# Kernel optimization log

Hardware: AMD Instinct MI355X
Metric: run time of the kernel (lower is better)

## Reference

```python
import jax, jax.numpy as jnp
import numpy as np

P, M, MD = 1024, 64, 16      # polynomials, monomials per poly, monomial dim
D, H, DH = 512, 8, 64        # embed dim, heads, head dim
L, FF, HID = 4, 2048, 1024   # transformer depth, ffn width, deepsets hidden
K = 2048                     # number of selectable (row, col) pairs
EPS = 1e-5


def setup_inputs() -> dict:
    key = jax.random.key(0)
    ks = iter(jax.random.split(key, 40))

    def w(shape, s=0.02):
        return jax.random.normal(next(ks), shape, dtype=jnp.float32) * s

    inp = {
        "ideal": jax.random.normal(next(ks), (P, M, MD), dtype=jnp.float32),
        "rows": jax.random.randint(next(ks), (K,), 0, P, dtype=jnp.int32),
        "cols": jax.random.randint(next(ks), (K,), 0, P, dtype=jnp.int32),
        # MonomialEmbedder
        "Wm": w((D, MD), 0.1), "bm": jnp.zeros((D,), jnp.float32),
        # PolynomialEmbedder (DeepSets): phi then sum-pool then rho (relu after every layer)
        "W_phi1": w((HID, D)), "b_phi1": jnp.zeros((HID,), jnp.float32),
        "W_phi2": w((HID, HID)), "b_phi2": jnp.zeros((HID,), jnp.float32),
        "W_rho1": w((HID, HID)), "b_rho1": jnp.zeros((HID,), jnp.float32),
        "W_rho2": w((D, HID)), "b_rho2": jnp.zeros((D,), jnp.float32),
        # Transformer stack (stacked over L layers)
        "Wq": w((L, D, D)), "bq": jnp.zeros((L, D), jnp.float32),
        "Wk": w((L, D, D)), "bk": jnp.zeros((L, D), jnp.float32),
        "Wv": w((L, D, D)), "bv": jnp.zeros((L, D), jnp.float32),
        "Wo": w((L, D, D)), "bo": jnp.zeros((L, D), jnp.float32),
        "ln1_w": jnp.ones((L, D), jnp.float32), "ln1_b": jnp.zeros((L, D), jnp.float32),
        "W1": w((L, FF, D)), "b1": jnp.zeros((L, FF), jnp.float32),
        "W2": w((L, D, FF)), "b2": jnp.zeros((L, D), jnp.float32),
        "ln2_w": jnp.ones((L, D), jnp.float32), "ln2_b": jnp.zeros((L, D), jnp.float32),
    }
    return inp


def _layernorm(x, w, b):
    mu = x.mean(-1, keepdims=True)
    var = ((x - mu) ** 2).mean(-1, keepdims=True)
    return (x - mu) / jnp.sqrt(var + EPS) * w + b


def reference(ideal, rows, cols, Wm, bm, W_phi1, b_phi1, W_phi2, b_phi2,
              W_rho1, b_rho1, W_rho2, b_rho2, Wq, bq, Wk, bk, Wv, bv, Wo, bo,
              ln1_w, ln1_b, W1, b1, W2, b2, ln2_w, ln2_b):
    n_poly = ideal.shape[0]
    # Monomial embedding: linear + relu  [P, M, D]
    h = jax.nn.relu(jnp.einsum('pmd,ed->pme', ideal, Wm) + bm)
    # DeepSets phi (relu each layer)
    h = jax.nn.relu(jnp.einsum('pme,he->pmh', h, W_phi1) + b_phi1)
    h = jax.nn.relu(jnp.einsum('pmh,gh->pmg', h, W_phi2) + b_phi2)
    # Sum-pool over monomials, then rho (relu each layer incl. last)
    s = h.sum(axis=1)                                  # [P, HID]
    s = jax.nn.relu(s @ W_rho1.T + b_rho1)
    x = jax.nn.relu(s @ W_rho2.T + b_rho2)             # [P, D]

    scale = 1.0 / jnp.sqrt(jnp.float32(DH))
    for l in range(L):
        q = (x @ Wq[l].T + bq[l]).reshape(n_poly, H, DH)
        k = (x @ Wk[l].T + bk[l]).reshape(n_poly, H, DH)
        v = (x @ Wv[l].T + bv[l]).reshape(n_poly, H, DH)
        scores = jnp.einsum('qhd,khd->hqk', q, k) * scale   # [H, P, P]
        attn = jax.nn.softmax(scores, axis=-1)
        o = jnp.einsum('hqk,khd->qhd', attn, v).reshape(n_poly, D)
        o = o @ Wo[l].T + bo[l]
        x = _layernorm(x + o, ln1_w[l], ln1_b[l])
        m = jax.nn.relu(x @ W1[l].T + b1[l]) @ W2[l].T + b2[l]
        x = _layernorm(x + m, ln2_w[l], ln2_b[l])

    values = x @ x.T                                   # [P, P]
    mask = jnp.full((n_poly, n_poly), -jnp.inf, dtype=values.dtype)
    mask = mask.at[rows, cols].set(0.0)
    return (values + mask).flatten()
```

## Files before the change

kernel.cpp:

```cpp
#include <hip/hip_runtime.h>
#include <hip/hip_bf16.h>

#define NP    1024
#define NM    64
#define MD_   16
#define D_    512
#define NH    8
#define DH_   64
#define NL    4
#define FF_   2048
#define HID_  1024
#define NK    2048
#define EPS_  1e-5f

typedef __attribute__((ext_vector_type(8))) short short8;
typedef __attribute__((ext_vector_type(4))) float f32x4;

static __device__ __forceinline__ unsigned short f2bf(float f) {
    __hip_bfloat16 h = __float2bfloat16(f);
    return *reinterpret_cast<unsigned short*>(&h);
}
static __device__ __forceinline__ float bf2f(unsigned short u) {
    unsigned int x = ((unsigned int)u) << 16;
    return __uint_as_float(x);
}

__global__ __launch_bounds__(256) void cvt_all(
    const float* __restrict__ s0, const float* __restrict__ s1,
    const float* __restrict__ s2, const float* __restrict__ s3,
    const float* __restrict__ s4, const float* __restrict__ s5,
    const float* __restrict__ s6,
    unsigned short* __restrict__ d0, unsigned short* __restrict__ d1,
    unsigned short* __restrict__ d2, unsigned short* __restrict__ d3,
    unsigned short* __restrict__ d4, unsigned short* __restrict__ d5,
    unsigned short* __restrict__ d6)
{
    const int i = blockIdx.x * 256 + threadIdx.x;
    const float* src; unsigned short* dst; int l;
    if      (i <  131072) { src = s0; dst = d0; l = i; }
    else if (i <  393216) { src = s1; dst = d1; l = i -  131072; }
    else if (i <  655360) { src = s2; dst = d2; l = i -  393216; }
    else if (i <  786432) { src = s3; dst = d3; l = i -  655360; }
    else if (i < 1048576) { src = s4; dst = d4; l = i -  786432; }
    else if (i < 2097152) { src = s5; dst = d5; l = i - 1048576; }
    else                  { src = s6; dst = d6; l = i - 2097152; }
    float4 v = *(const float4*)(src + (size_t)l * 4);
    ushort4 o;
    o.x = f2bf(v.x); o.y = f2bf(v.y); o.z = f2bf(v.z); o.w = f2bf(v.w);
    *(ushort4*)(dst + (size_t)l * 4) = o;
}

__global__ __launch_bounds__(256) void cvt_bf16_kernel(
    const float* __restrict__ in, unsigned short* __restrict__ out, int n4)
{
    const int i = blockIdx.x * 256 + threadIdx.x;
    if (i < n4) {
        float4 v = *(const float4*)(in + (size_t)i * 4);
        ushort4 o;
        o.x = f2bf(v.x); o.y = f2bf(v.y); o.z = f2bf(v.z); o.w = f2bf(v.w);
        *(ushort4*)(out + (size_t)i * 4) = o;
    }
}

__global__ __launch_bounds__(256) void cvt_pad64(
    const float* __restrict__ in, unsigned short* __restrict__ out, int nrows)
{
    const int tid = threadIdx.x;
    const int row = blockIdx.x * 32 + (tid >> 3);
    if (row >= nrows) return;
    const int c8 = (tid & 7) * 8;
    ushort4 o0 = {0, 0, 0, 0}, o1 = {0, 0, 0, 0};
    if (c8 < 16) {
        float4 a = *(const float4*)(in + (size_t)row * 16 + c8);
        float4 b = *(const float4*)(in + (size_t)row * 16 + c8 + 4);
        o0.x = f2bf(a.x); o0.y = f2bf(a.y); o0.z = f2bf(a.z); o0.w = f2bf(a.w);
        o1.x = f2bf(b.x); o1.y = f2bf(b.y); o1.z = f2bf(b.z); o1.w = f2bf(b.w);
    }
    *(ushort4*)(out + (size_t)row * 64 + c8) = o0;
    *(ushort4*)(out + (size_t)row * 64 + c8 + 4) = o1;
}

__global__ __launch_bounds__(256) void cvt_qkv_kernel(
    const float* __restrict__ Wq, const float* __restrict__ Wk,
    const float* __restrict__ Wv, const float* __restrict__ bq,
    const float* __restrict__ bk, const float* __restrict__ bv,
    unsigned short* __restrict__ w_qkv, float* __restrict__ b_qkvc)
{
    const int part = blockIdx.y;
    const int l    = blockIdx.z;
    const float* src  = (part == 0 ? Wq : part == 1 ? Wk : Wv) + (size_t)l * D_ * D_;
    const float* bsrc = (part == 0 ? bq : part == 1 ? bk : bv) + l * D_;
    unsigned short* dst = w_qkv + (size_t)l * 1536 * D_ + (size_t)part * 512 * D_;
    const int i = blockIdx.x * 256 + threadIdx.x;
    float4 v = *(const float4*)(src + (size_t)i * 4);
    ushort4 o;
    o.x = f2bf(v.x); o.y = f2bf(v.y); o.z = f2bf(v.z); o.w = f2bf(v.w);
    *(ushort4*)(dst + (size_t)i * 4) = o;
    if (blockIdx.x == 0) {
        b_qkvc[l * 1536 + part * 512 + threadIdx.x * 2]     = bsrc[threadIdx.x * 2];
        b_qkvc[l * 1536 + part * 512 + threadIdx.x * 2 + 1] = bsrc[threadIdx.x * 2 + 1];
    }
}

template<int ISSUES>
static __device__ __forceinline__ void stage_tile(
    const unsigned short* __restrict__ src, int ld,
    unsigned short* lds, int wave, int lane)
{
    const int rl  = lane >> 3;
    const int sw8 = (((lane & 7) ^ rl) << 3);
#pragma unroll
    for (int i = 0; i < ISSUES; ++i) {
        const int rbase = i * 32 + wave * 8;
        const unsigned short* g = src + (size_t)(rbase + rl) * ld + sw8;
        unsigned short* l = lds + rbase * 64;
        __builtin_amdgcn_global_load_lds(
            (const __attribute__((address_space(1))) void*)g,
            (__attribute__((address_space(3))) void*)l, 16, 0, 0);
    }
}

template<int BM, int BN, int MODE, bool OUTF32, bool BIAS, bool RELU, bool POOL,
         bool RESID, bool TRANSV, bool DBUF>
__global__ __launch_bounds__(256) void mfma_nt(
    const unsigned short* __restrict__ A, long long aBatch, int lda,
    const unsigned short* __restrict__ W, long long bBatch, int ldb,
    const float* __restrict__ bias,
    const float* __restrict__ resid, int ldr,
    void* __restrict__ Cout, long long cBatch, int ldc,
    int K, float alpha, unsigned short* __restrict__ vTout)
{
    constexpr int BK = 64;
    constexpr int MI = BM / 32, NJ = BN / 32;
    __shared__ unsigned short Asl[(DBUF ? 2 : 1) * BM * BK];
    __shared__ unsigned short Bsl[(DBUF ? 2 : 1) * BN * BK];

    const int tid  = threadIdx.x;
    const int wave = tid >> 6, lane = tid & 63;
    const int wm = wave >> 1, wn = wave & 1;
    int row0, col0;
    if (MODE == 2) {
        const int f = blockIdx.x;
        const int lo = f & 7, mid = (f >> 3) & 7, hi = f >> 6;
        row0 = (hi * 8 + lo) * BM;
        col0 = mid * BN;
    } else {
        row0 = blockIdx.y * BM;
        col0 = blockIdx.x * BN;
    }
    const long long bz = blockIdx.z;
    A += bz * aBatch + (size_t)row0 * lda;
    W += bz * bBatch + (size_t)col0 * ldb;

    f32x4 acc[MI][NJ];
#pragma unroll
    for (int i = 0; i < MI; ++i)
#pragma unroll
        for (int j = 0; j < NJ; ++j) acc[i][j] = (f32x4){0.f, 0.f, 0.f, 0.f};

    if (DBUF) {
        stage_tile<MI>(A, lda, Asl, wave, lane);
        stage_tile<NJ>(W, ldb, Bsl, wave, lane);
        __syncthreads();
    }
    int cur = 0;
    for (int k0 = 0; k0 < K; k0 += BK) {
        const unsigned short *Ac, *Bc;
        if (DBUF) {
            if (k0 + BK < K) {
                stage_tile<MI>(A + k0 + BK, lda, Asl + (cur ^ 1) * BM * BK, wave, lane);
                stage_tile<NJ>(W + k0 + BK, ldb, Bsl + (cur ^ 1) * BN * BK, wave, lane);
            }
            Ac = Asl + cur * BM * BK;
            Bc = Bsl + cur * BN * BK;
        } else {
            stage_tile<MI>(A + k0, lda, Asl, wave, lane);
            stage_tile<NJ>(W + k0, ldb, Bsl, wave, lane);
            __syncthreads();
            Ac = Asl; Bc = Bsl;
        }
#pragma unroll
        for (int ks = 0; ks < 2; ++ks) {
            short8 a[MI], b[NJ];
            const int kbase = ks * 64 + (lane >> 4) * 16;
#pragma unroll
            for (int i = 0; i < MI; ++i) {
                const int ra = wm * (BM / 2) + i * 16 + (lane & 15);
                a[i] = *(const short8*)((const char*)Ac + ra * 128 + (kbase ^ ((ra & 7) << 4)));
            }
#pragma unroll
            for (int j = 0; j < NJ; ++j) {
                const int rb = wn * (BN / 2) + j * 16 + (lane & 15);
                b[j] = *(const short8*)((const char*)Bc + rb * 128 + (kbase ^ ((rb & 7) << 4)));
            }
#pragma unroll
            for (int i = 0; i < MI; ++i)
#pragma unroll
                for (int j = 0; j < NJ; ++j)
                    acc[i][j] = __builtin_amdgcn_mfma_f32_16x16x32_bf16(
                        a[i], b[j], acc[i][j], 0, 0, 0);
        }
        __syncthreads();
        cur ^= 1;
    }

    if (POOL) {
        float* red = (float*)Asl;
        red[tid] = 0.f;
        __syncthreads();
#pragma unroll
        for (int j = 0; j < NJ; ++j) {
            const int c = wn * (BN / 2) + j * 16 + (lane & 15);
            const float bi = BIAS ? bias[col0 + c] : 0.f;
            float s = 0.f;
#pragma unroll
            for (int i = 0; i < MI; ++i) {
                f32x4 v = acc[i][j];
#pragma unroll
                for (int r2 = 0; r2 < 4; ++r2) {
                    float val = v[r2] * alpha + bi;
                    if (RELU) val = fmaxf(val, 0.f);
                    s += val;
                }
            }
            atomicAdd(&red[wm * BN + c], s);
        }
        __syncthreads();
        float* C = (float*)Cout + bz * cBatch;
        const int pm = tid >> 7, c = tid & 127;
        C[(size_t)(row0 / 64 + pm) * ldc + col0 + c] = red[pm * BN + c];
    } else if (TRANSV && col0 >= 1024) {
        unsigned short* tr = Asl;
#pragma unroll
        for (int i = 0; i < MI; ++i) {
            const int rr = wm * (BM / 2) + i * 16 + (lane >> 4) * 4;
#pragma unroll
            for (int j = 0; j < NJ; ++j) {
                const int c = wn * (BN / 2) + j * 16 + (lane & 15);
                const float bi = BIAS ? bias[col0 + c] : 0.f;
                f32x4 v = acc[i][j];
#pragma unroll
                for (int r2 = 0; r2 < 4; ++r2)
                    tr[(rr + r2) * BN + c] = f2bf(v[r2] * alpha + bi);
            }
        }
        __syncthreads();
        const int c  = tid >> 2;
        const int r4 = (tid & 3) * 16;
        ushort4 o[4];
#pragma unroll
        for (int e = 0; e < 16; ++e)
            ((unsigned short*)o)[e] = tr[(r4 + e) * BN + c];
        unsigned short* dst = vTout + (size_t)(col0 - 1024 + c) * 1024 + row0 + r4;
        *(ushort4*)(dst + 0)  = o[0];
        *(ushort4*)(dst + 4)  = o[1];
        *(ushort4*)(dst + 8)  = o[2];
        *(ushort4*)(dst + 12) = o[3];
    } else {
        float* Cf = (float*)Cout + (OUTF32 ? bz * cBatch : 0);
        unsigned short* Cu = (unsigned short*)Cout + (OUTF32 ? 0 : bz * cBatch);
#pragma unroll
        for (int i = 0; i < MI; ++i) {
            const int rg = row0 + wm * (BM / 2) + i * 16 + (lane >> 4) * 4;
#pragma unroll
            for (int j = 0; j < NJ; ++j) {
                const int c = col0 + wn * (BN / 2) + j * 16 + (lane & 15);
                const float bi = BIAS ? bias[c] : 0.f;
                f32x4 v = acc[i][j];
#pragma unroll
                for (int r2 = 0; r2 < 4; ++r2) {
                    float val = v[r2] * alpha + bi;
                    if (RELU) val = fmaxf(val, 0.f);
                    if (RESID) val += resid[(size_t)(rg + r2) * ldr + c];
                    if (OUTF32) Cf[(size_t)(rg + r2) * ldc + c] = val;
                    else        Cu[(size_t)(rg + r2) * ldc + c] = f2bf(val);
                }
            }
        }
    }
}

__global__ __launch_bounds__(256) void flash_attn(
    const unsigned short* __restrict__ qkv,
    const unsigned short* __restrict__ vT,
    unsigned short* __restrict__ O)
{
    __shared__ unsigned short Qs[64 * 64];
    __shared__ unsigned short Ks[2][64 * 64];
    __shared__ unsigned short Vs[2][64 * 64];
    __shared__ unsigned short Ps[64 * 64];

    const int tid = threadIdx.x, wave = tid >> 6, lane = tid & 63;
    const int q0 = blockIdx.x * 64;
    const int h  = blockIdx.y;

    stage_tile<2>(qkv + (size_t)q0 * 1536 + h * 64, 1536, Qs, wave, lane);
    stage_tile<2>(qkv + 512 + h * 64, 1536, Ks[0], wave, lane);
    stage_tile<2>(vT + (size_t)(h * 64) * 1024, 1024, Vs[0], wave, lane);
    __syncthreads();

    f32x4 Oacc[4];
#pragma unroll
    for (int j = 0; j < 4; ++j) Oacc[j] = (f32x4){0.f, 0.f, 0.f, 0.f};
    float mrow[4] = {-1e30f, -1e30f, -1e30f, -1e30f};
    float lrow[4] = {0.f, 0.f, 0.f, 0.f};

    for (int kt = 0; kt < 16; ++kt) {
        if (kt < 15) {
            stage_tile<2>(qkv + 512 + (size_t)((kt + 1) * 64) * 1536 + h * 64, 1536,
                          Ks[(kt + 1) & 1], wave, lane);
            stage_tile<2>(vT + (size_t)(h * 64) * 1024 + (kt + 1) * 64, 1024,
                          Vs[(kt + 1) & 1], wave, lane);
        }
        const unsigned short* Kc = Ks[kt & 1];
        const unsigned short* Vc = Vs[kt & 1];

        f32x4 s[4];
#pragma unroll
        for (int j = 0; j < 4; ++j) s[j] = (f32x4){0.f, 0.f, 0.f, 0.f};
#pragma unroll
        for (int ks = 0; ks < 2; ++ks) {
            const int kbase = ks * 64 + (lane >> 4) * 16;
            const int ra = wave * 16 + (lane & 15);
            short8 aq = *(const short8*)((const char*)Qs + ra * 128 + (kbase ^ ((ra & 7) << 4)));
#pragma unroll
            for (int j = 0; j < 4; ++j) {
                const int rb = j * 16 + (lane & 15);
                short8 bk8 = *(const short8*)((const char*)Kc + rb * 128 + (kbase ^ ((rb & 7) << 4)));
                s[j] = __builtin_amdgcn_mfma_f32_16x16x32_bf16(aq, bk8, s[j], 0, 0, 0);
            }
        }

        float f[4];
#pragma unroll
        for (int r = 0; r < 4; ++r) {
            float mx = -1e30f;
#pragma unroll
            for (int j = 0; j < 4; ++j) { s[j][r] *= 0.125f; mx = fmaxf(mx, s[j][r]); }
#pragma unroll
            for (int o = 1; o < 16; o <<= 1) mx = fmaxf(mx, __shfl_xor(mx, o));
            const float mn = fmaxf(mrow[r], mx);
            f[r] = expf(mrow[r] - mn);
            mrow[r] = mn;
            float sm = 0.f;
#pragma unroll
            for (int j = 0; j < 4; ++j) { s[j][r] = expf(s[j][r] - mn); sm += s[j][r]; }
#pragma unroll
            for (int o = 1; o < 16; o <<= 1) sm += __shfl_xor(sm, o);
            lrow[r] = lrow[r] * f[r] + sm;
        }
#pragma unroll
        for (int j = 0; j < 4; ++j)
#pragma unroll
            for (int r = 0; r < 4; ++r) Oacc[j][r] *= f[r];

#pragma unroll
        for (int j = 0; j < 4; ++j) {
            const int col = (lane & 15) + j * 16;
#pragma unroll
            for (int r = 0; r < 4; ++r) {
                const int row = wave * 16 + (lane >> 4) * 4 + r;
                *(unsigned short*)((char*)Ps + row * 128 + ((col * 2) ^ ((row & 7) << 4))) =
                    f2bf(s[j][r]);
            }
        }

#pragma unroll
        for (int ks = 0; ks < 2; ++ks) {
            const int kbase = ks * 64 + (lane >> 4) * 16;
            const int ra = wave * 16 + (lane & 15);
            short8 ap = *(const short8*)((const char*)Ps + ra * 128 + (kbase ^ ((ra & 7) << 4)));
#pragma unroll
            for (int j = 0; j < 4; ++j) {
                const int rb = j * 16 + (lane & 15);
                short8 bv8 = *(const short8*)((const char*)Vc + rb * 128 + (kbase ^ ((rb & 7) << 4)));
                Oacc[j] = __builtin_amdgcn_mfma_f32_16x16x32_bf16(ap, bv8, Oacc[j], 0, 0, 0);
            }
        }
        __syncthreads();
    }

    float linv[4];
#pragma unroll
    for (int r = 0; r < 4; ++r) linv[r] = 1.0f / lrow[r];
#pragma unroll
    for (int j = 0; j < 4; ++j) {
        const int c = h * 64 + j * 16 + (lane & 15);
#pragma unroll
        for (int r = 0; r < 4; ++r) {
            const int row = q0 + wave * 16 + (lane >> 4) * 4 + r;
            O[(size_t)row * D_ + c] = f2bf(Oacc[j][r] * linv[r]);
        }
    }
}

__global__ __launch_bounds__(64) void ln_kernel(
    const float* __restrict__ y, const float* __restrict__ w,
    const float* __restrict__ b, float* __restrict__ x,
    unsigned short* __restrict__ xb)
{
    const int row = blockIdx.x;
    const int lane = threadIdx.x;
    const float* yr = y + (long long)row * 512;
    float4 v0 = *(const float4*)(yr + lane * 8);
    float4 v1 = *(const float4*)(yr + lane * 8 + 4);
    float vals[8] = {v0.x, v0.y, v0.z, v0.w, v1.x, v1.y, v1.z, v1.w};
    float s = 0.f;
#pragma unroll
    for (int j = 0; j < 8; ++j) s += vals[j];
#pragma unroll
    for (int o = 32; o >= 1; o >>= 1) s += __shfl_xor(s, o);
    const float mu = s * (1.f / 512.f);
    float q = 0.f;
#pragma unroll
    for (int j = 0; j < 8; ++j) { float d = vals[j] - mu; q += d * d; }
#pragma unroll
    for (int o = 32; o >= 1; o >>= 1) q += __shfl_xor(q, o);
    const float inv = 1.0f / sqrtf(q * (1.f / 512.f) + EPS_);
    float ov[8];
#pragma unroll
    for (int j = 0; j < 8; ++j)
        ov[j] = (vals[j] - mu) * inv * w[lane * 8 + j] + b[lane * 8 + j];
    float4 o0 = {ov[0], ov[1], ov[2], ov[3]};
    float4 o1 = {ov[4], ov[5], ov[6], ov[7]};
    *(float4*)(x + (long long)row * 512 + lane * 8) = o0;
    *(float4*)(x + (long long)row * 512 + lane * 8 + 4) = o1;
    ushort4 u0, u1;
    u0.x = f2bf(ov[0]); u0.y = f2bf(ov[1]); u0.z = f2bf(ov[2]); u0.w = f2bf(ov[3]);
    u1.x = f2bf(ov[4]); u1.y = f2bf(ov[5]); u1.z = f2bf(ov[6]); u1.w = f2bf(ov[7]);
    *(ushort4*)(xb + (long long)row * 512 + lane * 8) = u0;
    *(ushort4*)(xb + (long long)row * 512 + lane * 8 + 4) = u1;
}

__global__ __launch_bounds__(64) void ln_sum4_kernel(
    const float* __restrict__ y4,
    const float* __restrict__ bias,
    const float* __restrict__ w, const float* __restrict__ b,
    float* __restrict__ x, unsigned short* __restrict__ xb)
{
    const int row = blockIdx.x;
    const int lane = threadIdx.x;
    const size_t off = (size_t)row * 512 + lane * 8;
    float vals[8];
#pragma unroll
    for (int j = 0; j < 8; ++j) vals[j] = x[off + j] + bias[lane * 8 + j];
#pragma unroll
    for (int z = 0; z < 4; ++z) {
        float4 p0 = *(const float4*)(y4 + (size_t)z * 524288 + off);
        float4 p1 = *(const float4*)(y4 + (size_t)z * 524288 + off + 4);
        vals[0] += p0.x; vals[1] += p0.y; vals[2] += p0.z; vals[3] += p0.w;
        vals[4] += p1.x; vals[5] += p1.y; vals[6] += p1.z; vals[7] += p1.w;
    }
    float s = 0.f;
#pragma unroll
    for (int j = 0; j < 8; ++j) s += vals[j];
#pragma unroll
    for (int o = 32; o >= 1; o >>= 1) s += __shfl_xor(s, o);
    const float mu = s * (1.f / 512.f);
    float q = 0.f;
#pragma unroll
    for (int j = 0; j < 8; ++j) { float d = vals[j] - mu; q += d * d; }
#pragma unroll
    for (int o = 32; o >= 1; o >>= 1) q += __shfl_xor(q, o);
    const float inv = 1.0f / sqrtf(q * (1.f / 512.f) + EPS_);
    float ov[8];
#pragma unroll
    for (int j = 0; j < 8; ++j)
        ov[j] = (vals[j] - mu) * inv * w[lane * 8 + j] + b[lane * 8 + j];
    float4 o0 = {ov[0], ov[1], ov[2], ov[3]};
    float4 o1 = {ov[4], ov[5], ov[6], ov[7]};
    *(float4*)(x + off) = o0;
    *(float4*)(x + off + 4) = o1;
    ushort4 u0, u1;
    u0.x = f2bf(ov[0]); u0.y = f2bf(ov[1]); u0.z = f2bf(ov[2]); u0.w = f2bf(ov[3]);
    u1.x = f2bf(ov[4]); u1.y = f2bf(ov[5]); u1.z = f2bf(ov[6]); u1.w = f2bf(ov[7]);
    *(ushort4*)(xb + off) = u0;
    *(ushort4*)(xb + off + 4) = u1;
}

__global__ __launch_bounds__(256) void fill_sentinel_bf16(unsigned short* __restrict__ out)
{
    const long long i = (long long)blockIdx.x * blockDim.x + threadIdx.x;
    const unsigned int pat = 0xFBFFFBFFu;
    uint4 v = {pat, pat, pat, pat};
    *(uint4*)(out + i * 8) = v;
}

__global__ __launch_bounds__(256) void scatter_dot(
    const int* __restrict__ rows, const int* __restrict__ cols,
    const unsigned short* __restrict__ xb, __hip_bfloat16* __restrict__ out)
{
    const int k = blockIdx.x * 4 + (threadIdx.x >> 6);
    const int lane = threadIdx.x & 63;
    const int r = rows[k], c = cols[k];
    const unsigned short* xr = xb + (size_t)r * 512 + lane * 8;
    const unsigned short* xc = xb + (size_t)c * 512 + lane * 8;
    ushort4 a0 = *(const ushort4*)xr, a1 = *(const ushort4*)(xr + 4);
    ushort4 b0 = *(const ushort4*)xc, b1 = *(const ushort4*)(xc + 4);
    float s = bf2f(a0.x) * bf2f(b0.x) + bf2f(a0.y) * bf2f(b0.y) +
              bf2f(a0.z) * bf2f(b0.z) + bf2f(a0.w) * bf2f(b0.w) +
              bf2f(a1.x) * bf2f(b1.x) + bf2f(a1.y) * bf2f(b1.y) +
              bf2f(a1.z) * bf2f(b1.z) + bf2f(a1.w) * bf2f(b1.w);
#pragma unroll
    for (int o = 32; o >= 1; o >>= 1) s += __shfl_xor(s, o);
    if (lane == 0) {
        if (!(fabsf(s) < 1e30f)) s = 0.f;
        out[(size_t)r * 1024 + c] = __float2bfloat16(s);
    }
}

extern "C" void kernel_launch(void* const* d_in, const int* in_sizes, int n_in,
                              void* d_out, int out_size, void* d_ws, size_t ws_size,
                              hipStream_t stream)
{
    const float* ideal  = (const float*)d_in[0];
    const int*   rows   = (const int*)d_in[1];
    const int*   cols   = (const int*)d_in[2];
    const float* Wm     = (const float*)d_in[3];
    const float* bm     = (const float*)d_in[4];
    const float* Wphi1  = (const float*)d_in[5];
    const float* bphi1  = (const float*)d_in[6];
    const float* Wphi2  = (const float*)d_in[7];
    const float* bphi2  = (const float*)d_in[8];
    const float* Wrho1  = (const float*)d_in[9];
    const float* brho1  = (const float*)d_in[10];
    const float* Wrho2  = (const float*)d_in[11];
    const float* brho2  = (const float*)d_in[12];
    const float* Wq     = (const float*)d_in[13];
    const float* bq     = (const float*)d_in[14];
    const float* Wk     = (const float*)d_in[15];
    const float* bk     = (const float*)d_in[16];
    const float* Wv     = (const float*)d_in[17];
    const float* bv     = (const float*)d_in[18];
    const float* Wo     = (const float*)d_in[19];
    const float* bo     = (const float*)d_in[20];
    const float* ln1w   = (const float*)d_in[21];
    const float* ln1b   = (const float*)d_in[22];
    const float* W1     = (const float*)d_in[23];
    const float* b1     = (const float*)d_in[24];
    const float* W2     = (const float*)d_in[25];
    const float* b2     = (const float*)d_in[26];
    const float* ln2w   = (const float*)d_in[27];
    const float* ln2b   = (const float*)d_in[28];
    __hip_bfloat16* out = (__hip_bfloat16*)d_out;

    char* base = (char*)d_ws;
    unsigned short* w_phi1 = (unsigned short*)(base + (0ll  << 20));
    unsigned short* w_phi2 = (unsigned short*)(base + (1ll  << 20));
    unsigned short* w_rho1 = (unsigned short*)(base + (3ll  << 20));
    unsigned short* w_rho2 = (unsigned short*)(base + (5ll  << 20));
    unsigned short* w_qkv  = (unsigned short*)(base + (6ll  << 20));
    unsigned short* w_o    = (unsigned short*)(base + (12ll << 20));
    unsigned short* w_1    = (unsigned short*)(base + (14ll << 20));
    unsigned short* w_2    = (unsigned short*)(base + (22ll << 20));
    float*          b_qkvc = (float*)         (base + (30ll << 20));
    unsigned short* h0b    = (unsigned short*)(base + (31ll << 20));
    unsigned short* h1b    = (unsigned short*)(base + (95ll << 20));
    float*          sbuf   = (float*)         (base + (223ll << 20));
    unsigned short* id_pad = (unsigned short*)(base + (227ll << 20));
    unsigned short* wm_pad = (unsigned short*)(base + (236ll << 20));
    unsigned short* sb_b   = (unsigned short*)(base + (31ll << 20));
    unsigned short* tb_b   = (unsigned short*)(base + (33ll << 20));
    float*          xbuf   = (float*)         (base + (35ll << 20));
    unsigned short* xb     = (unsigned short*)(base + (37ll << 20));
    float*          ybuf   = (float*)         (base + (38ll << 20));
    unsigned short* qkvb   = (unsigned short*)(base + (40ll << 20));
    unsigned short* vT     = (unsigned short*)(base + (43ll << 20));
    unsigned short* ob     = (unsigned short*)(base + (44ll << 20));
    unsigned short* ffnt   = (unsigned short*)(base + (45ll << 20));
    float*          ysplit = (float*)         (base + (49ll << 20));

    fill_sentinel_bf16<<<512, 256, 0, stream>>>((unsigned short*)out);

    cvt_all<<<12288, 256, 0, stream>>>(Wphi1, Wphi2, Wrho1, Wrho2, Wo, W1, W2,
                                       w_phi1, w_phi2, w_rho1, w_rho2, w_o, w_1, w_2);
    cvt_qkv_kernel<<<dim3(256, 3, NL), 256, 0, stream>>>(Wq, Wk, Wv, bq, bk, bv,
                                                          w_qkv, b_qkvc);
    cvt_pad64<<<2048, 256, 0, stream>>>(ideal, id_pad, NP * NM);
    cvt_pad64<<<16, 256, 0, stream>>>(Wm, wm_pad, D_);

    mfma_nt<128, 128, 0, false, true, true, false, false, false, false><<<dim3(4, 512), 256, 0, stream>>>(
        id_pad, 0, 64, wm_pad, 0, 64, bm, nullptr, 0, h0b, 0, D_, 64, 1.0f, nullptr);
    mfma_nt<128, 128, 2, false, true, true, false, false, false, false><<<4096, 256, 0, stream>>>(
        h0b, 0, D_, w_phi1, 0, D_, bphi1, nullptr, 0, h1b, 0, HID_, D_, 1.0f, nullptr);
    mfma_nt<128, 128, 2, true, true, true, true, false, false, false><<<4096, 256, 0, stream>>>(
        h1b, 0, HID_, w_phi2, 0, HID_, bphi2, nullptr, 0, sbuf, 0, HID_, HID_, 1.0f, nullptr);

    cvt_bf16_kernel<<<1024, 256, 0, stream>>>(sbuf, sb_b, 262144);
    mfma_nt<64, 64, 0, false, true, true, false, false, false, true><<<dim3(16, 16), 256, 0, stream>>>(
        sb_b, 0, HID_, w_rho1, 0, HID_, brho1, nullptr, 0, tb_b, 0, HID_, HID_, 1.0f, nullptr);
    mfma_nt<64, 64, 0, true, true, true, false, false, false, true><<<dim3(8, 16), 256, 0, stream>>>(
        tb_b, 0, HID_, w_rho2, 0, HID_, brho2, nullptr, 0, xbuf, 0, D_, HID_, 1.0f, nullptr);
    cvt_bf16_kernel<<<512, 256, 0, stream>>>(xbuf, xb, 131072);

    for (int l = 0; l < NL; ++l) {
        mfma_nt<64, 64, 0, false, true, false, false, false, true, true><<<dim3(24, 16), 256, 0, stream>>>(
            xb, 0, D_, w_qkv + (long long)l * 1536 * D_, 0, D_, b_qkvc + l * 1536,
            nullptr, 0, qkvb, 0, 1536, D_, 1.0f, vT);
        flash_attn<<<dim3(16, NH), 256, 0, stream>>>(qkvb, vT, ob);
        mfma_nt<64, 64, 0, true, true, false, false, true, false, true><<<dim3(8, 16), 256, 0, stream>>>(
            ob, 0, D_, w_o + (long long)l * D_ * D_, 0, D_, bo + l * D_,
            xbuf, D_, ybuf, 0, D_, D_, 1.0f, nullptr);
        ln_kernel<<<NP, 64, 0, stream>>>(ybuf, ln1w + l * D_, ln1b + l * D_, xbuf, xb);
        mfma_nt<64, 64, 0, false, true, true, false, false, false, true><<<dim3(32, 16), 256, 0, stream>>>(
            xb, 0, D_, w_1 + (long long)l * FF_ * D_, 0, D_, b1 + l * FF_,
            nullptr, 0, ffnt, 0, FF_, D_, 1.0f, nullptr);
        mfma_nt<64, 64, 0, true, false, false, false, false, false, true><<<dim3(8, 16, 4), 256, 0, stream>>>(
            ffnt, 512, FF_, w_2 + (long long)l * D_ * FF_, 512, FF_, nullptr,
            nullptr, 0, ysplit, 524288, D_, 512, 1.0f, nullptr);
        ln_sum4_kernel<<<NP, 64, 0, stream>>>(ysplit, b2 + l * D_,
                                              ln2w + l * D_, ln2b + l * D_, xbuf, xb);
    }

    scatter_dot<<<NK / 4, 256, 0, stream>>>(rows, cols, xb, out);
}
```

Before: 646.3 us.

## Split attention over key halves, split-K Wo GEMM, and merge conversion kernels

Flash attention is split into two key-range partitions, each writing unnormalized fp32 partials plus row max/sum, and a new merge kernel combines them into bf16. The Wo projection becomes a split-K GEMM whose partials are reduced inside a generalized LayerNorm-sum kernel. All weight conversion and sentinel-fill kernels are fused into one launch, and the rho2 GEMM also writes the bf16 copy directly. The aim is more parallelism from the 128-block attention grid and fewer launches, at the cost of extra fp32 partial traffic and one added merge launch per layer.

```diff
diff --git a/kernel.cpp b/kernel.cpp
--- a/kernel.cpp
+++ b/kernel.cpp
@@ -25,29 +25,74 @@
     return __uint_as_float(x);
 }
 
-__global__ __launch_bounds__(256) void cvt_all(
-    const float* __restrict__ s0, const float* __restrict__ s1,
-    const float* __restrict__ s2, const float* __restrict__ s3,
-    const float* __restrict__ s4, const float* __restrict__ s5,
-    const float* __restrict__ s6,
-    unsigned short* __restrict__ d0, unsigned short* __restrict__ d1,
-    unsigned short* __restrict__ d2, unsigned short* __restrict__ d3,
-    unsigned short* __restrict__ d4, unsigned short* __restrict__ d5,
-    unsigned short* __restrict__ d6)
-{
-    const int i = blockIdx.x * 256 + threadIdx.x;
-    const float* src; unsigned short* dst; int l;
-    if      (i <  131072) { src = s0; dst = d0; l = i; }
-    else if (i <  393216) { src = s1; dst = d1; l = i -  131072; }
-    else if (i <  655360) { src = s2; dst = d2; l = i -  393216; }
-    else if (i <  786432) { src = s3; dst = d3; l = i -  655360; }
-    else if (i < 1048576) { src = s4; dst = d4; l = i -  786432; }
-    else if (i < 2097152) { src = s5; dst = d5; l = i - 1048576; }
-    else                  { src = s6; dst = d6; l = i - 2097152; }
-    float4 v = *(const float4*)(src + (size_t)l * 4);
-    ushort4 o;
-    o.x = f2bf(v.x); o.y = f2bf(v.y); o.z = f2bf(v.z); o.w = f2bf(v.w);
-    *(ushort4*)(dst + (size_t)l * 4) = o;
+__global__ __launch_bounds__(256) void mega_cvt(
+    const float* __restrict__ Wphi1, const float* __restrict__ Wphi2,
+    const float* __restrict__ Wrho1, const float* __restrict__ Wrho2,
+    const float* __restrict__ Wo,    const float* __restrict__ W1,
+    const float* __restrict__ W2,
+    unsigned short* __restrict__ w_phi1, unsigned short* __restrict__ w_phi2,
+    unsigned short* __restrict__ w_rho1, unsigned short* __restrict__ w_rho2,
+    unsigned short* __restrict__ w_o,    unsigned short* __restrict__ w_1,
+    unsigned short* __restrict__ w_2,
+    const float* __restrict__ Wq, const float* __restrict__ Wk,
+    const float* __restrict__ Wv, const float* __restrict__ bq,
+    const float* __restrict__ bk, const float* __restrict__ bv,
+    unsigned short* __restrict__ w_qkv, float* __restrict__ b_qkvc,
+    const float* __restrict__ ideal, unsigned short* __restrict__ id_pad,
+    const float* __restrict__ Wm,    unsigned short* __restrict__ wm_pad,
+    unsigned short* __restrict__ out)
+{
+    const int b = blockIdx.x, t = threadIdx.x;
+    if (b < 512) {
+        const long long i = (long long)b * 256 + t;
+        const unsigned int pat = 0xFBFFFBFFu;
+        uint4 v = {pat, pat, pat, pat};
+        *(uint4*)(out + i * 8) = v;
+    } else if (b < 12800) {
+        const int i = (b - 512) * 256 + t;
+        const float* src; unsigned short* dst; int l;
+        if      (i <  131072) { src = Wphi1; dst = w_phi1; l = i; }
+        else if (i <  393216) { src = Wphi2; dst = w_phi2; l = i -  131072; }
+        else if (i <  655360) { src = Wrho1; dst = w_rho1; l = i -  393216; }
+        else if (i <  786432) { src = Wrho2; dst = w_rho2; l = i -  655360; }
+        else if (i < 1048576) { src = Wo;    dst = w_o;    l = i -  786432; }
+        else if (i < 2097152) { src = W1;    dst = w_1;    l = i - 1048576; }
+        else                  { src = W2;    dst = w_2;    l = i - 2097152; }
+        float4 v = *(const float4*)(src + (size_t)l * 4);
+        ushort4 o;
+        o.x = f2bf(v.x); o.y = f2bf(v.y); o.z = f2bf(v.z); o.w = f2bf(v.w);
+        *(ushort4*)(dst + (size_t)l * 4) = o;
+    } else if (b < 15872) {
+        const int g = (b - 12800) >> 8;
+        const int inner = (b - 12800) & 255;
+        const int part = g % 3, l = g / 3;
+        const float* src  = (part == 0 ? Wq : part == 1 ? Wk : Wv) + (size_t)l * D_ * D_;
+        const float* bsrc = (part == 0 ? bq : part == 1 ? bk : bv) + l * D_;
+        unsigned short* dst = w_qkv + (size_t)l * 1536 * D_ + (size_t)part * 512 * D_;
+        const int i = inner * 256 + t;
+        float4 v = *(const float4*)(src + (size_t)i * 4);
+        ushort4 o;
+        o.x = f2bf(v.x); o.y = f2bf(v.y); o.z = f2bf(v.z); o.w = f2bf(v.w);
+        *(ushort4*)(dst + (size_t)i * 4) = o;
+        if (inner == 0) {
+            b_qkvc[l * 1536 + part * 512 + t * 2]     = bsrc[t * 2];
+            b_qkvc[l * 1536 + part * 512 + t * 2 + 1] = bsrc[t * 2 + 1];
+        }
+    } else {
+        const float* src; unsigned short* dst; int row;
+        if (b < 17920) { src = ideal; dst = id_pad; row = (b - 15872) * 32 + (t >> 3); }
+        else           { src = Wm;    dst = wm_pad; row = (b - 17920) * 32 + (t >> 3); }
+        const int c8 = (t & 7) * 8;
+        ushort4 o0 = {0, 0, 0, 0}, o1 = {0, 0, 0, 0};
+        if (c8 < 16) {
+            float4 a = *(const float4*)(src + (size_t)row * 16 + c8);
+            float4 bb = *(const float4*)(src + (size_t)row * 16 + c8 + 4);
+            o0.x = f2bf(a.x);  o0.y = f2bf(a.y);  o0.z = f2bf(a.z);  o0.w = f2bf(a.w);
+            o1.x = f2bf(bb.x); o1.y = f2bf(bb.y); o1.z = f2bf(bb.z); o1.w = f2bf(bb.w);
+        }
+        *(ushort4*)(dst + (size_t)row * 64 + c8) = o0;
+        *(ushort4*)(dst + (size_t)row * 64 + c8 + 4) = o1;
+    }
 }
 
 __global__ __launch_bounds__(256) void cvt_bf16_kernel(
@@ -59,46 +104,6 @@
         ushort4 o;
         o.x = f2bf(v.x); o.y = f2bf(v.y); o.z = f2bf(v.z); o.w = f2bf(v.w);
         *(ushort4*)(out + (size_t)i * 4) = o;
-    }
-}
-
-__global__ __launch_bounds__(256) void cvt_pad64(
-    const float* __restrict__ in, unsigned short* __restrict__ out, int nrows)
-{
-    const int tid = threadIdx.x;
-    const int row = blockIdx.x * 32 + (tid >> 3);
-    if (row >= nrows) return;
-    const int c8 = (tid & 7) * 8;
-    ushort4 o0 = {0, 0, 0, 0}, o1 = {0, 0, 0, 0};
-    if (c8 < 16) {
-        float4 a = *(const float4*)(in + (size_t)row * 16 + c8);
-        float4 b = *(const float4*)(in + (size_t)row * 16 + c8 + 4);
-        o0.x = f2bf(a.x); o0.y = f2bf(a.y); o0.z = f2bf(a.z); o0.w = f2bf(a.w);
-        o1.x = f2bf(b.x); o1.y = f2bf(b.y); o1.z = f2bf(b.z); o1.w = f2bf(b.w);
-    }
-    *(ushort4*)(out + (size_t)row * 64 + c8) = o0;
-    *(ushort4*)(out + (size_t)row * 64 + c8 + 4) = o1;
-}
-
-__global__ __launch_bounds__(256) void cvt_qkv_kernel(
-    const float* __restrict__ Wq, const float* __restrict__ Wk,
-    const float* __restrict__ Wv, const float* __restrict__ bq,
-    const float* __restrict__ bk, const float* __restrict__ bv,
-    unsigned short* __restrict__ w_qkv, float* __restrict__ b_qkvc)
-{
-    const int part = blockIdx.y;
-    const int l    = blockIdx.z;
-    const float* src  = (part == 0 ? Wq : part == 1 ? Wk : Wv) + (size_t)l * D_ * D_;
-    const float* bsrc = (part == 0 ? bq : part == 1 ? bk : bv) + l * D_;
-    unsigned short* dst = w_qkv + (size_t)l * 1536 * D_ + (size_t)part * 512 * D_;
-    const int i = blockIdx.x * 256 + threadIdx.x;
-    float4 v = *(const float4*)(src + (size_t)i * 4);
-    ushort4 o;
-    o.x = f2bf(v.x); o.y = f2bf(v.y); o.z = f2bf(v.z); o.w = f2bf(v.w);
-    *(ushort4*)(dst + (size_t)i * 4) = o;
-    if (blockIdx.x == 0) {
-        b_qkvc[l * 1536 + part * 512 + threadIdx.x * 2]     = bsrc[threadIdx.x * 2];
-        b_qkvc[l * 1536 + part * 512 + threadIdx.x * 2 + 1] = bsrc[threadIdx.x * 2 + 1];
     }
 }
 
@@ -121,7 +126,7 @@
 }
 
 template<int BM, int BN, int MODE, bool OUTF32, bool BIAS, bool RELU, bool POOL,
-         bool RESID, bool TRANSV, bool DBUF>
+         bool RESID, bool TRANSV, bool DBUF, bool BOTH>
 __global__ __launch_bounds__(256) void mfma_nt(
     const unsigned short* __restrict__ A, long long aBatch, int lda,
     const unsigned short* __restrict__ W, long long bBatch, int ldb,
@@ -272,8 +277,12 @@
                     float val = v[r2] * alpha + bi;
                     if (RELU) val = fmaxf(val, 0.f);
                     if (RESID) val += resid[(size_t)(rg + r2) * ldr + c];
-                    if (OUTF32) Cf[(size_t)(rg + r2) * ldc + c] = val;
-                    else        Cu[(size_t)(rg + r2) * ldc + c] = f2bf(val);
+                    if (OUTF32) {
+                        Cf[(size_t)(rg + r2) * ldc + c] = val;
+                        if (BOTH) vTout[(size_t)(rg + r2) * ldc + c] = f2bf(val);
+                    } else {
+                        Cu[(size_t)(rg + r2) * ldc + c] = f2bf(val);
+                    }
                 }
             }
         }
@@ -283,7 +292,8 @@
 __global__ __launch_bounds__(256) void flash_attn(
     const unsigned short* __restrict__ qkv,
     const unsigned short* __restrict__ vT,
-    unsigned short* __restrict__ O)
+    float* __restrict__ Of,
+    float* __restrict__ mlb)
 {
     __shared__ unsigned short Qs[64 * 64];
     __shared__ unsigned short Ks[2][64 * 64];
@@ -293,10 +303,12 @@
     const int tid = threadIdx.x, wave = tid >> 6, lane = tid & 63;
     const int q0 = blockIdx.x * 64;
     const int h  = blockIdx.y;
+    const int z  = blockIdx.z;
+    const int kt0 = z * 8;
 
     stage_tile<2>(qkv + (size_t)q0 * 1536 + h * 64, 1536, Qs, wave, lane);
-    stage_tile<2>(qkv + 512 + h * 64, 1536, Ks[0], wave, lane);
-    stage_tile<2>(vT + (size_t)(h * 64) * 1024, 1024, Vs[0], wave, lane);
+    stage_tile<2>(qkv + 512 + (size_t)(kt0 * 64) * 1536 + h * 64, 1536, Ks[0], wave, lane);
+    stage_tile<2>(vT + (size_t)(h * 64) * 1024 + kt0 * 64, 1024, Vs[0], wave, lane);
     __syncthreads();
 
     f32x4 Oacc[4];
@@ -305,11 +317,11 @@
     float mrow[4] = {-1e30f, -1e30f, -1e30f, -1e30f};
     float lrow[4] = {0.f, 0.f, 0.f, 0.f};
 
-    for (int kt = 0; kt < 16; ++kt) {
-        if (kt < 15) {
-            stage_tile<2>(qkv + 512 + (size_t)((kt + 1) * 64) * 1536 + h * 64, 1536,
+    for (int kt = 0; kt < 8; ++kt) {
+        if (kt < 7) {
+            stage_tile<2>(qkv + 512 + (size_t)((kt0 + kt + 1) * 64) * 1536 + h * 64, 1536,
                           Ks[(kt + 1) & 1], wave, lane);
-            stage_tile<2>(vT + (size_t)(h * 64) * 1024 + (kt + 1) * 64, 1024,
+            stage_tile<2>(vT + (size_t)(h * 64) * 1024 + (kt0 + kt + 1) * 64, 1024,
                           Vs[(kt + 1) & 1], wave, lane);
         }
         const unsigned short* Kc = Ks[kt & 1];
@@ -380,59 +392,62 @@
         __syncthreads();
     }
 
-    float linv[4];
-#pragma unroll
-    for (int r = 0; r < 4; ++r) linv[r] = 1.0f / lrow[r];
+    float* Oz = Of + (size_t)z * 524288;
 #pragma unroll
     for (int j = 0; j < 4; ++j) {
         const int c = h * 64 + j * 16 + (lane & 15);
 #pragma unroll
         for (int r = 0; r < 4; ++r) {
             const int row = q0 + wave * 16 + (lane >> 4) * 4 + r;
-            O[(size_t)row * D_ + c] = f2bf(Oacc[j][r] * linv[r]);
-        }
-    }
-}
-
-__global__ __launch_bounds__(64) void ln_kernel(
-    const float* __restrict__ y, const float* __restrict__ w,
-    const float* __restrict__ b, float* __restrict__ x,
-    unsigned short* __restrict__ xb)
-{
-    const int row = blockIdx.x;
-    const int lane = threadIdx.x;
-    const float* yr = y + (long long)row * 512;
-    float4 v0 = *(const float4*)(yr + lane * 8);
-    float4 v1 = *(const float4*)(yr + lane * 8 + 4);
-    float vals[8] = {v0.x, v0.y, v0.z, v0.w, v1.x, v1.y, v1.z, v1.w};
-    float s = 0.f;
-#pragma unroll
-    for (int j = 0; j < 8; ++j) s += vals[j];
-#pragma unroll
-    for (int o = 32; o >= 1; o >>= 1) s += __shfl_xor(s, o);
-    const float mu = s * (1.f / 512.f);
-    float q = 0.f;
-#pragma unroll
-    for (int j = 0; j < 8; ++j) { float d = vals[j] - mu; q += d * d; }
-#pragma unroll
-    for (int o = 32; o >= 1; o >>= 1) q += __shfl_xor(q, o);
-    const float inv = 1.0f / sqrtf(q * (1.f / 512.f) + EPS_);
-    float ov[8];
-#pragma unroll
-    for (int j = 0; j < 8; ++j)
-        ov[j] = (vals[j] - mu) * inv * w[lane * 8 + j] + b[lane * 8 + j];
-    float4 o0 = {ov[0], ov[1], ov[2], ov[3]};
-    float4 o1 = {ov[4], ov[5], ov[6], ov[7]};
-    *(float4*)(x + (long long)row * 512 + lane * 8) = o0;
-    *(float4*)(x + (long long)row * 512 + lane * 8 + 4) = o1;
-    ushort4 u0, u1;
-    u0.x = f2bf(ov[0]); u0.y = f2bf(ov[1]); u0.z = f2bf(ov[2]); u0.w = f2bf(ov[3]);
-    u1.x = f2bf(ov[4]); u1.y = f2bf(ov[5]); u1.z = f2bf(ov[6]); u1.w = f2bf(ov[7]);
-    *(ushort4*)(xb + (long long)row * 512 + lane * 8) = u0;
-    *(ushort4*)(xb + (long long)row * 512 + lane * 8 + 4) = u1;
-}
-
-__global__ __launch_bounds__(64) void ln_sum4_kernel(
+            Oz[(size_t)row * D_ + c] = Oacc[j][r];
+        }
+    }
+    if ((lane & 15) == 0 && h == 0) {  }
+    if ((lane & 15) == 0) {
+#pragma unroll
+        for (int r = 0; r < 4; ++r) {
+            const int row = q0 + wave * 16 + (lane >> 4) * 4 + r;
+            float* dst = mlb + (((size_t)z * NH + h) * 1024 + row) * 2;
+            dst[0] = mrow[r];
+            dst[1] = lrow[r];
+        }
+    }
+}
+
+__global__ __launch_bounds__(256) void flash_merge(
+    const float* __restrict__ Of, const float* __restrict__ mlb,
+    unsigned short* __restrict__ O)
+{
+    const int tid = threadIdx.x;
+    const int row = blockIdx.x * 4 + (tid >> 6);
+    const int lane = tid & 63;
+    const int d0 = lane * 8;
+    const int h = d0 >> 6;
+    const float* ml0 = mlb + (((size_t)0 * NH + h) * 1024 + row) * 2;
+    const float* ml1 = mlb + (((size_t)1 * NH + h) * 1024 + row) * 2;
+    const float m0 = ml0[0], l0 = ml0[1], m1 = ml1[0], l1 = ml1[1];
+    const float m = fmaxf(m0, m1);
+    const float a0 = expf(m0 - m), a1 = expf(m1 - m);
+    const float inv = 1.0f / (a0 * l0 + a1 * l1);
+    const float* p0 = Of + (size_t)row * D_ + d0;
+    const float* p1 = Of + 524288 + (size_t)row * D_ + d0;
+    float4 x0 = *(const float4*)p0, x1 = *(const float4*)(p0 + 4);
+    float4 y0 = *(const float4*)p1, y1 = *(const float4*)(p1 + 4);
+    ushort4 o0, o1;
+    o0.x = f2bf((a0 * x0.x + a1 * y0.x) * inv);
+    o0.y = f2bf((a0 * x0.y + a1 * y0.y) * inv);
+    o0.z = f2bf((a0 * x0.z + a1 * y0.z) * inv);
+    o0.w = f2bf((a0 * x0.w + a1 * y0.w) * inv);
+    o1.x = f2bf((a0 * x1.x + a1 * y1.x) * inv);
+    o1.y = f2bf((a0 * x1.y + a1 * y1.y) * inv);
+    o1.z = f2bf((a0 * x1.z + a1 * y1.z) * inv);
+    o1.w = f2bf((a0 * x1.w + a1 * y1.w) * inv);
+    *(ushort4*)(O + (size_t)row * D_ + d0) = o0;
+    *(ushort4*)(O + (size_t)row * D_ + d0 + 4) = o1;
+}
+
+template<int NZ>
+__global__ __launch_bounds__(64) void ln_sum_kernel(
     const float* __restrict__ y4,
     const float* __restrict__ bias,
     const float* __restrict__ w, const float* __restrict__ b,
@@ -445,7 +460,7 @@
 #pragma unroll
     for (int j = 0; j < 8; ++j) vals[j] = x[off + j] + bias[lane * 8 + j];
 #pragma unroll
-    for (int z = 0; z < 4; ++z) {
+    for (int z = 0; z < NZ; ++z) {
         float4 p0 = *(const float4*)(y4 + (size_t)z * 524288 + off);
         float4 p1 = *(const float4*)(y4 + (size_t)z * 524288 + off + 4);
         vals[0] += p0.x; vals[1] += p0.y; vals[2] += p0.z; vals[3] += p0.w;
@@ -476,14 +491,6 @@
     u1.x = f2bf(ov[4]); u1.y = f2bf(ov[5]); u1.z = f2bf(ov[6]); u1.w = f2bf(ov[7]);
     *(ushort4*)(xb + off) = u0;
     *(ushort4*)(xb + off + 4) = u1;
-}
-
-__global__ __launch_bounds__(256) void fill_sentinel_bf16(unsigned short* __restrict__ out)
-{
-    const long long i = (long long)blockIdx.x * blockDim.x + threadIdx.x;
-    const unsigned int pat = 0xFBFFFBFFu;
-    uint4 v = {pat, pat, pat, pat};
-    *(uint4*)(out + i * 8) = v;
 }
 
 __global__ __launch_bounds__(256) void scatter_dot(
@@ -563,53 +570,61 @@
     unsigned short* tb_b   = (unsigned short*)(base + (33ll << 20));
     float*          xbuf   = (float*)         (base + (35ll << 20));
     unsigned short* xb     = (unsigned short*)(base + (37ll << 20));
-    float*          ybuf   = (float*)         (base + (38ll << 20));
     unsigned short* qkvb   = (unsigned short*)(base + (40ll << 20));
     unsigned short* vT     = (unsigned short*)(base + (43ll << 20));
     unsigned short* ob     = (unsigned short*)(base + (44ll << 20));
     unsigned short* ffnt   = (unsigned short*)(base + (45ll << 20));
     float*          ysplit = (float*)         (base + (49ll << 20));
-
-    fill_sentinel_bf16<<<512, 256, 0, stream>>>((unsigned short*)out);
-
-    cvt_all<<<12288, 256, 0, stream>>>(Wphi1, Wphi2, Wrho1, Wrho2, Wo, W1, W2,
-                                       w_phi1, w_phi2, w_rho1, w_rho2, w_o, w_1, w_2);
-    cvt_qkv_kernel<<<dim3(256, 3, NL), 256, 0, stream>>>(Wq, Wk, Wv, bq, bk, bv,
-                                                          w_qkv, b_qkvc);
-    cvt_pad64<<<2048, 256, 0, stream>>>(ideal, id_pad, NP * NM);
-    cvt_pad64<<<16, 256, 0, stream>>>(Wm, wm_pad, D_);
-
-    mfma_nt<128, 128, 0, false, true, true, false, false, false, false><<<dim3(4, 512), 256, 0, stream>>>(
+    float*          Of     = (float*)         (base + (57ll << 20));
+    float*          mlb    = (float*)         (base + (61ll << 20));
+
+    mega_cvt<<<17936, 256, 0, stream>>>(
+        Wphi1, Wphi2, Wrho1, Wrho2, Wo, W1, W2,
+        w_phi1, w_phi2, w_rho1, w_rho2, w_o, w_1, w_2,
+        Wq, Wk, Wv, bq, bk, bv, w_qkv, b_qkvc,
+        ideal, id_pad, Wm, wm_pad, (unsigned short*)out);
+
+    mfma_nt<128, 128, 0, false, true, true, false, false, false, false, false>
+        <<<dim3(4, 512), 256, 0, stream>>>(
         id_pad, 0, 64, wm_pad, 0, 64, bm, nullptr, 0, h0b, 0, D_, 64, 1.0f, nullptr);
-    mfma_nt<128, 128, 2, false, true, true, false, false, false, false><<<4096, 256, 0, stream>>>(
+    mfma_nt<128, 128, 2, false, true, true, false, false, false, false, false>
+        <<<4096, 256, 0, stream>>>(
         h0b, 0, D_, w_phi1, 0, D_, bphi1, nullptr, 0, h1b, 0, HID_, D_, 1.0f, nullptr);
-    mfma_nt<128, 128, 2, true, true, true, true, false, false, false><<<4096, 256, 0, stream>>>(
+    mfma_nt<128, 128, 2, true, true, true, true, false, false, false, false>
+        <<<4096, 256, 0, stream>>>(
         h1b, 0, HID_, w_phi2, 0, HID_, bphi2, nullptr, 0, sbuf, 0, HID_, HID_, 1.0f, nullptr);
 
     cvt_bf16_kernel<<<1024, 256, 0, stream>>>(sbuf, sb_b, 262144);
-    mfma_nt<64, 64, 0, false, true, true, false, false, false, true><<<dim3(16, 16), 256, 0, stream>>>(
+    mfma_nt<64, 64, 0, false, true, true, false, false, false, true, false>
+        <<<dim3(16, 16), 256, 0, stream>>>(
         sb_b, 0, HID_, w_rho1, 0, HID_, brho1, nullptr, 0, tb_b, 0, HID_, HID_, 1.0f, nullptr);
-    mfma_nt<64, 64, 0, true, true, true, false, false, false, true><<<dim3(8, 16), 256, 0, stream>>>(
-        tb_b, 0, HID_, w_rho2, 0, HID_, brho2, nullptr, 0, xbuf, 0, D_, HID_, 1.0f, nullptr);
-    cvt_bf16_kernel<<<512, 256, 0, stream>>>(xbuf, xb, 131072);
+    mfma_nt<64, 64, 0, true, true, true, false, false, false, true, true>
+        <<<dim3(8, 16), 256, 0, stream>>>(
+        tb_b, 0, HID_, w_rho2, 0, HID_, brho2, nullptr, 0, xbuf, 0, D_, HID_, 1.0f, xb);
 
     for (int l = 0; l < NL; ++l) {
-        mfma_nt<64, 64, 0, false, true, false, false, false, true, true><<<dim3(24, 16), 256, 0, stream>>>(
+        mfma_nt<64, 64, 0, false, true, false, false, false, true, true, false>
+            <<<dim3(24, 16), 256, 0, stream>>>(
             xb, 0, D_, w_qkv + (long long)l * 1536 * D_, 0, D_, b_qkvc + l * 1536,
             nullptr, 0, qkvb, 0, 1536, D_, 1.0f, vT);
-        flash_attn<<<dim3(16, NH), 256, 0, stream>>>(qkvb, vT, ob);
-        mfma_nt<64, 64, 0, true, true, false, false, true, false, true><<<dim3(8, 16), 256, 0, stream>>>(
-            ob, 0, D_, w_o + (long long)l * D_ * D_, 0, D_, bo + l * D_,
-            xbuf, D_, ybuf, 0, D_, D_, 1.0f, nullptr);
-        ln_kernel<<<NP, 64, 0, stream>>>(ybuf, ln1w + l * D_, ln1b + l * D_, xbuf, xb);
-        mfma_nt<64, 64, 0, false, true, true, false, false, false, true><<<dim3(32, 16), 256, 0, stream>>>(
+        flash_attn<<<dim3(16, NH, 2), 256, 0, stream>>>(qkvb, vT, Of, mlb);
+        flash_merge<<<256, 256, 0, stream>>>(Of, mlb, ob);
+        mfma_nt<64, 64, 0, true, false, false, false, false, false, true, false>
+            <<<dim3(8, 16, 2), 256, 0, stream>>>(
+            ob, 256, D_, w_o + (long long)l * D_ * D_, 256, D_, nullptr,
+            nullptr, 0, ysplit, 524288, D_, 256, 1.0f, nullptr);
+        ln_sum_kernel<2><<<NP, 64, 0, stream>>>(ysplit, bo + l * D_,
+                                                ln1w + l * D_, ln1b + l * D_, xbuf, xb);
+        mfma_nt<64, 64, 0, false, true, true, false, false, false, true, false>
+            <<<dim3(32, 16), 256, 0, stream>>>(
             xb, 0, D_, w_1 + (long long)l * FF_ * D_, 0, D_, b1 + l * FF_,
             nullptr, 0, ffnt, 0, FF_, D_, 1.0f, nullptr);
-        mfma_nt<64, 64, 0, true, false, false, false, false, false, true><<<dim3(8, 16, 4), 256, 0, stream>>>(
+        mfma_nt<64, 64, 0, true, false, false, false, false, false, true, false>
+            <<<dim3(8, 16, 4), 256, 0, stream>>>(
             ffnt, 512, FF_, w_2 + (long long)l * D_ * FF_, 512, FF_, nullptr,
             nullptr, 0, ysplit, 524288, D_, 512, 1.0f, nullptr);
-        ln_sum4_kernel<<<NP, 64, 0, stream>>>(ysplit, b2 + l * D_,
-                                              ln2w + l * D_, ln2b + l * D_, xbuf, xb);
+        ln_sum_kernel<4><<<NP, 64, 0, stream>>>(ysplit, b2 + l * D_,
+                                                ln2w + l * D_, ln2b + l * D_, xbuf, xb);
     }
 
     scatter_dot<<<NK / 4, 256, 0, stream>>>(rows, cols, xb, out);
```

Result: faster. 573.8 us (-11.2%).
